# Optimization experiments

Hardware: AMD Instinct MI355X
Metric: run time of the kernel (lower is better)

## Reference

```python
import jax, jax.numpy as jnp
import numpy as np

N, M, KLEN, D_MODEL, H = 256, 256, 128, 256, 8
DK = D_MODEL // H


def _linear_params(key, out_dim, in_dim):
    # torch nn.Linear default init: U(-1/sqrt(in), 1/sqrt(in))
    kw, kb = jax.random.split(key)
    bound = 1.0 / np.sqrt(in_dim)
    W = jax.random.uniform(kw, (out_dim, in_dim), jnp.float32, -bound, bound)
    b = jax.random.uniform(kb, (out_dim,), jnp.float32, -bound, bound)
    return W, b


def setup_inputs() -> dict:
    key = jax.random.key(0)
    ks = jax.random.split(key, 7)
    query = jax.random.normal(ks[0], (N, D_MODEL), jnp.float32)
    key_t = jax.random.normal(ks[1], (M, KLEN, D_MODEL), jnp.float32)
    value = jax.random.normal(ks[2], (M, KLEN, D_MODEL), jnp.float32)
    Wq, bq = _linear_params(ks[3], D_MODEL, D_MODEL)
    Wk, bk = _linear_params(ks[4], D_MODEL, D_MODEL)
    Wv, bv = _linear_params(ks[5], D_MODEL, D_MODEL)
    Wo, bo = _linear_params(ks[6], D_MODEL, D_MODEL)
    return {"query": query, "key": key_t, "value": value,
            "Wq": Wq, "bq": bq, "Wk": Wk, "bk": bk,
            "Wv": Wv, "bv": bv, "Wo": Wo, "bo": bo}


def reference(query, key, value, Wq, bq, Wk, bk, Wv, bv, Wo, bo):
    n = query.shape[0]
    m = key.shape[0]
    # projections (torch Linear: x @ W.T + b)
    q = (query @ Wq.T + bq).reshape(n, H, DK)                      # [n,h,d]
    k = (key @ Wk.T + bk).reshape(m, -1, H, DK).transpose(0, 2, 1, 3)   # [m,h,k,d]
    v = (value @ Wv.T + bv).reshape(m, -1, H, DK).transpose(0, 2, 1, 3)  # [m,h,k,d]
    # cross-batch attention scores: [n,m,h,k]
    scores = jnp.einsum('nhd,mhkd->nmhk', q, k) / np.sqrt(DK).astype(np.float32)
    p_attn = jax.nn.softmax(scores, axis=-1)
    # context: [n,m,h,d] -> [n,m,d_model]
    ctx = jnp.einsum('nmhk,mhkd->nmhd', p_attn, v).reshape(n, m, H * DK)
    return ctx @ Wo.T + bo
```

## Files before the change

kernel.cpp:

```cpp
#include <hip/hip_runtime.h>


typedef unsigned short u16;
typedef unsigned int u32;
typedef __attribute__((ext_vector_type(8))) _Float16 half8;
typedef __attribute__((ext_vector_type(4))) _Float16 half4;
typedef __attribute__((ext_vector_type(4))) float f32x4;
typedef __attribute__((ext_vector_type(4))) unsigned short us4;
typedef __attribute__((ext_vector_type(2))) unsigned int u32x2;

__device__ __forceinline__ u16 f2h(float v) {
  _Float16 h = (_Float16)v;
  return __builtin_bit_cast(u16, h);
}
__device__ __forceinline__ u32 pk2(float lo, float hi) {
  return (u32)f2h(lo) | ((u32)f2h(hi) << 16);
}
__device__ __forceinline__ f32x4 mf16(half8 a, half8 b, f32x4 c) {
  return __builtin_amdgcn_mfma_f32_16x16x32_f16(a, b, c, 0, 0, 0);
}
__device__ __forceinline__ f32x4 mf16k16(half4 a, half4 b, f32x4 c) {
  return __builtin_amdgcn_mfma_f32_16x16x16f16(a, b, c, 0, 0, 0);
}
__device__ __forceinline__ void gload_lds16(const void* g, void* l) {
  __builtin_amdgcn_global_load_lds((const __attribute__((address_space(1))) u32*)g,
                                   (__attribute__((address_space(3))) u32*)l, 16, 0, 0);
}

template<int MODE>
__global__ __launch_bounds__(256) void proj_kernel(const float* __restrict__ X,
                                                   const float* __restrict__ W,
                                                   const float* __restrict__ bias,
                                                   u16* __restrict__ out,
                                                   const float* __restrict__ Wo,
                                                   u16* __restrict__ wof) {
  if (MODE == 0 && blockIdx.x >= 16) {
    int t = (blockIdx.x - 16) * 256 + threadIdx.x;
    int ln = t & 63, jtile = (t >> 6) & 15, h = t >> 10;
    int j = jtile * 16 + (ln & 15);
    int d0 = h * 32 + (ln >> 4) * 8;
    float4 g0 = *(const float4*)(Wo + j * 256 + d0);
    float4 g1 = *(const float4*)(Wo + j * 256 + d0 + 4);
    us4 h0 = { f2h(g0.x), f2h(g0.y), f2h(g0.z), f2h(g0.w) };
    us4 h1 = { f2h(g1.x), f2h(g1.y), f2h(g1.z), f2h(g1.w) };
    *(us4*)(wof + t * 8) = h0;
    *(us4*)(wof + t * 8 + 4) = h1;
    return;
  }
  __shared__ __align__(16) u16 xa[64 * 256];
  __shared__ __align__(16) u16 wa[64 * 256];
  int bid = blockIdx.x;
  int logical;
  if (MODE == 0) {
    logical = bid;
  } else {
    int chunk = gridDim.x >> 3;
    logical = (bid & 7) * chunk + (bid >> 3);
  }
  int rb = logical >> 2, cb = logical & 3;
  int tid = threadIdx.x;

  char* xb = (char*)xa;
  char* wb_ = (char*)wa;
#pragma unroll
  for (int i = 0; i < 16; ++i) {
    int idx = tid + i * 256;
    int row = idx >> 6, c4 = idx & 63;
    int so = (row * 512 + c4 * 8) ^ ((row & 7) << 4);
    float4 gx = *(const float4*)(X + (rb * 64 + row) * 256 + c4 * 4);
    us4 hx = { f2h(gx.x), f2h(gx.y), f2h(gx.z), f2h(gx.w) };
    *(us4*)(xb + so) = hx;
    float4 gw = *(const float4*)(W + (cb * 64 + row) * 256 + c4 * 4);
    us4 hw = { f2h(gw.x), f2h(gw.y), f2h(gw.z), f2h(gw.w) };
    *(us4*)(wb_ + so) = hw;
  }
  __syncthreads();

  int lane = tid & 63, w = tid >> 6;
  int lr = lane & 15, lq = lane >> 4;
  const char* ab = (MODE == 2) ? wb_ : xb;
  const char* bb = (MODE == 2) ? xb : wb_;

  half8 a[8];
#pragma unroll
  for (int kk = 0; kk < 8; ++kk)
    a[kk] = *(const half8*)(ab + (((w * 16 + lr) * 512 + kk * 64 + lq * 16) ^ ((lr & 7) << 4)));

#pragma unroll
  for (int ct = 0; ct < 4; ++ct) {
    f32x4 acc = {0.f, 0.f, 0.f, 0.f};
#pragma unroll
    for (int kk = 0; kk < 8; ++kk) {
      half8 b = *(const half8*)(bb + (((ct * 16 + lr) * 512 + kk * 64 + lq * 16) ^ ((lr & 7) << 4)));
      acc = mf16(a[kk], b, acc);
    }
    if (MODE != 2) {
      int j = cb * 64 + ct * 16 + lr;
      float bj = bias[j];
#pragma unroll
      for (int rr = 0; rr < 4; ++rr) {
        int gr = rb * 64 + w * 16 + lq * 4 + rr;
        float v = acc[rr] + bj;
        if (MODE == 0) {
          out[gr * 256 + j] = f2h(v);
        } else {
          int mm = gr >> 7, kl = gr & 127, hh = j >> 5, d = j & 31;
          out[(mm * 8 + hh) * 4096 + (kl >> 4) * 512 + ((d >> 3) * 16 + (kl & 15)) * 8 + (d & 7)] = f2h(v);
        }
      }
    } else {
#pragma unroll
      for (int rr = 0; rr < 4; ++rr) {
        int j = cb * 64 + w * 16 + lq * 4 + rr;
        float v = acc[rr] + bias[j];
        int gr = rb * 64 + ct * 16 + lr;
        int mm = gr >> 7, kl = gr & 127, hh = j >> 5, d = j & 31;
        int jt = d >> 4, lrp = d & 15, kt = kl >> 4, lqp = (kl >> 2) & 3, e = kl & 3;
        out[(((mm * 8 + hh) * 2 + jt) * 8 + kt) * 256 + (lqp * 16 + lrp) * 4 + e] = f2h(v);
      }
    }
  }
}

__global__ __launch_bounds__(512, 4) void fused_attn_kernel(const u16* __restrict__ qp,
                                                            const u16* __restrict__ kp,
                                                            const u16* __restrict__ vt3,
                                                            const u16* __restrict__ wof,
                                                            const float* __restrict__ bo,
                                                            float* __restrict__ out) {
  __shared__ __align__(16) u16 kbuf[2][4096];
  __shared__ __align__(16) u16 vbuf[2][4096];
  __shared__ __align__(16) u16 cbuf[2][4096];

  const int bid = blockIdx.x;
  const int xcd = bid & 7, idx = bid >> 3;
  const int m = xcd * 32 + (idx >> 1);
  const int nh = idx & 1;
  const int tid = threadIdx.x;
  const int w = tid >> 6, lane = tid & 63;
  const int lr = lane & 15, lq = lane >> 4;
  const int n0 = nh * 128 + w * 16;
  const float SCL2E = 0.25506980508f;

  const char* kg = (const char*)(kp + m * 8 * 4096);
  const char* vg = (const char*)(vt3 + m * 8 * 4096);

  gload_lds16(kg + w * 1024 + lane * 16, (char*)(&kbuf[0][0]) + w * 1024);
  gload_lds16(vg + w * 1024 + lane * 16, (char*)(&vbuf[0][0]) + w * 1024);
  __syncthreads();

  f32x4 accO[2][8];
#pragma unroll
  for (int jt = 0; jt < 2; ++jt)
#pragma unroll
    for (int nb = 0; nb < 8; ++nb) accO[jt][nb] = f32x4{0.f, 0.f, 0.f, 0.f};

  for (int h = 0; h < 8; ++h) {
    const int cur = h & 1;
    char* kb = (char*)(&kbuf[cur][0]);
    char* vb = (char*)(&vbuf[cur][0]);
    char* cb = (char*)(&cbuf[cur][0]);
    if (h < 7) {
      gload_lds16(kg + (h + 1) * 8192 + w * 1024 + lane * 16, (char*)(&kbuf[cur ^ 1][0]) + w * 1024);
      gload_lds16(vg + (h + 1) * 8192 + w * 1024 + lane * 16, (char*)(&vbuf[cur ^ 1][0]) + w * 1024);
    }
    half8 qa = *(const half8*)(qp + (n0 + lr) * 256 + h * 32 + lq * 8);
    f32x4 s[8];
    __builtin_amdgcn_s_setprio(1);
#pragma unroll
    for (int kt = 0; kt < 8; ++kt) {
      half8 ka = *(const half8*)(kb + kt * 1024 + lane * 16);
      f32x4 z = {0.f, 0.f, 0.f, 0.f};
      s[kt] = mf16(ka, qa, z);
    }
    __builtin_amdgcn_s_setprio(0);
    f32x4 m4 = s[0];
#pragma unroll
    for (int kt = 1; kt < 8; ++kt) {
      m4[0] = fmaxf(m4[0], s[kt][0]);
      m4[1] = fmaxf(m4[1], s[kt][1]);
      m4[2] = fmaxf(m4[2], s[kt][2]);
      m4[3] = fmaxf(m4[3], s[kt][3]);
    }
    float mx = fmaxf(fmaxf(m4[0], m4[1]), fmaxf(m4[2], m4[3]));
    mx = fmaxf(mx, __shfl_xor(mx, 16));
    mx = fmaxf(mx, __shfl_xor(mx, 32));
    float sA = 0.f, sB = 0.f;
    half4 pb[8];
#pragma unroll
    for (int kt = 0; kt < 8; ++kt) {
      float p0 = __builtin_amdgcn_exp2f((s[kt][0] - mx) * SCL2E);
      float p1 = __builtin_amdgcn_exp2f((s[kt][1] - mx) * SCL2E);
      float p2 = __builtin_amdgcn_exp2f((s[kt][2] - mx) * SCL2E);
      float p3 = __builtin_amdgcn_exp2f((s[kt][3] - mx) * SCL2E);
      sA += p0 + p1; sB += p2 + p3;
      u32x2 pw = { pk2(p0, p1), pk2(p2, p3) };
      pb[kt] = __builtin_bit_cast(half4, pw);
    }
    float sum = sA + sB;
    sum += __shfl_xor(sum, 16);
    sum += __shfl_xor(sum, 32);
    float inv = 1.0f / sum;
    f32x4 a0 = {0.f, 0.f, 0.f, 0.f}, a1 = {0.f, 0.f, 0.f, 0.f};
    __builtin_amdgcn_s_setprio(1);
#pragma unroll
    for (int kt = 0; kt < 8; ++kt) {
      half4 v0 = *(const half4*)(vb + kt * 512 + lane * 8);
      a0 = mf16k16(v0, pb[kt], a0);
      half4 v1 = *(const half4*)(vb + 4096 + kt * 512 + lane * 8);
      a1 = mf16k16(v1, pb[kt], a1);
    }
    __builtin_amdgcn_s_setprio(0);
    u32x2 c0 = { pk2(a0[0] * inv, a0[1] * inv), pk2(a0[2] * inv, a0[3] * inv) };
    u32x2 c1 = { pk2(a1[0] * inv, a1[1] * inv), pk2(a1[2] * inv, a1[3] * inv) };
    const int cwo = w * 1024 + ((lq >> 1) * 16 + lr) * 16 + (lq & 1) * 8;
    *(u32x2*)(cb + cwo) = c0;
    *(u32x2*)(cb + cwo + 512) = c1;
    __syncthreads();
    half8 wv0 = *(const half8*)(wof + ((h * 16 + w * 2 + 0) * 64 + lane) * 8);
    half8 wv1 = *(const half8*)(wof + ((h * 16 + w * 2 + 1) * 64 + lane) * 8);
    __builtin_amdgcn_s_setprio(1);
#pragma unroll
    for (int nb = 0; nb < 8; ++nb) {
      half8 cf = *(const half8*)(cb + nb * 1024 + lane * 16);
      accO[0][nb] = mf16(wv0, cf, accO[0][nb]);
      accO[1][nb] = mf16(wv1, cf, accO[1][nb]);
    }
    __builtin_amdgcn_s_setprio(0);
  }
#pragma unroll
  for (int jt = 0; jt < 2; ++jt) {
    const int j0 = w * 32 + jt * 16 + lq * 4;
    float4 bv = *(const float4*)(bo + j0);
#pragma unroll
    for (int nb = 0; nb < 8; ++nb) {
      const int n = nh * 128 + nb * 16 + lr;
      float4 r;
      r.x = accO[jt][nb][0] + bv.x;
      r.y = accO[jt][nb][1] + bv.y;
      r.z = accO[jt][nb][2] + bv.z;
      r.w = accO[jt][nb][3] + bv.w;
      *(float4*)(out + (n * 256 + m) * 256 + j0) = r;
    }
  }
}

extern "C" void kernel_launch(void* const* d_in, const int* in_sizes, int n_in,
                              void* d_out, int out_size, void* d_ws, size_t ws_size,
                              hipStream_t stream) {
  (void)in_sizes; (void)n_in; (void)out_size; (void)ws_size;
  const float* query = (const float*)d_in[0];
  const float* key   = (const float*)d_in[1];
  const float* value = (const float*)d_in[2];
  const float* Wq = (const float*)d_in[3];
  const float* bq = (const float*)d_in[4];
  const float* Wk = (const float*)d_in[5];
  const float* bk = (const float*)d_in[6];
  const float* Wv = (const float*)d_in[7];
  const float* bv = (const float*)d_in[8];
  const float* Wo = (const float*)d_in[9];
  const float* bo = (const float*)d_in[10];
  float* out = (float*)d_out;

  u16* ws = (u16*)d_ws;
  u16* kp  = ws;
  u16* vt3 = kp + 8388608;
  u16* qp  = vt3 + 8388608;
  u16* wof = qp + 65536;

  proj_kernel<0><<<48,   256, 0, stream>>>(query, Wq, bq, qp, Wo, wof);
  proj_kernel<1><<<2048, 256, 0, stream>>>(key,   Wk, bk, kp, nullptr, nullptr);
  proj_kernel<2><<<2048, 256, 0, stream>>>(value, Wv, bv, vt3, nullptr, nullptr);
  fused_attn_kernel<<<512, 512, 0, stream>>>(qp, kp, vt3, wof, bo, out);
}
```

Baseline: 85.79 us.

## Pre-convert weights to fp16 fragment layout in a separate kernel

A new kernel converts all four weight matrices to fp16 once, stored in MFMA fragment order. The projection kernels then read weight fragments straight from global memory instead of converting and staging a weight tile in LDS, which halves LDS use and allows higher occupancy. Outputs are written as vectorized 4-element stores in fragment layouts, including a fragment layout for Q. In the attention kernel, the Wo and Q fragment loads are hoisted earlier and the V loads are merged into one 16-byte read. This adds an extra kernel launch, and every block now rereads its weight fragments from global/L2.

```diff
diff --git a/kernel.cpp b/kernel.cpp
--- a/kernel.cpp
+++ b/kernel.cpp
@@ -27,41 +27,42 @@
                                    (__attribute__((address_space(3))) u32*)l, 16, 0, 0);
 }
 
+__global__ __launch_bounds__(256) void wcvt_kernel(const float* __restrict__ Wq,
+                                                   const float* __restrict__ Wk,
+                                                   const float* __restrict__ Wv,
+                                                   const float* __restrict__ Wo,
+                                                   u16* __restrict__ wfq, u16* __restrict__ wfk,
+                                                   u16* __restrict__ wfv, u16* __restrict__ wof) {
+  int t = blockIdx.x * 256 + threadIdx.x;
+  int widx = t >> 13, tl = t & 8191;
+  int ln = tl & 63, kk = (tl >> 6) & 7, jt = tl >> 9;
+  const float* src = widx == 0 ? Wq : widx == 1 ? Wk : widx == 2 ? Wv : Wo;
+  u16* dst = widx == 0 ? wfq : widx == 1 ? wfk : widx == 2 ? wfv : wof;
+  int j = jt * 16 + (ln & 15);
+  int k0 = kk * 32 + (ln >> 4) * 8;
+  float4 g0 = *(const float4*)(src + j * 256 + k0);
+  float4 g1 = *(const float4*)(src + j * 256 + k0 + 4);
+  us4 h0 = { f2h(g0.x), f2h(g0.y), f2h(g0.z), f2h(g0.w) };
+  us4 h1 = { f2h(g1.x), f2h(g1.y), f2h(g1.z), f2h(g1.w) };
+  int idx8 = (widx == 3) ? ((kk * 16 + jt) * 64 + ln)
+                         : ((jt * 8 + kk) * 64 + ln);
+  *(us4*)(dst + idx8 * 8) = h0;
+  *(us4*)(dst + idx8 * 8 + 4) = h1;
+}
+
 template<int MODE>
-__global__ __launch_bounds__(256) void proj_kernel(const float* __restrict__ X,
-                                                   const float* __restrict__ W,
-                                                   const float* __restrict__ bias,
-                                                   u16* __restrict__ out,
-                                                   const float* __restrict__ Wo,
-                                                   u16* __restrict__ wof) {
-  if (MODE == 0 && blockIdx.x >= 16) {
-    int t = (blockIdx.x - 16) * 256 + threadIdx.x;
-    int ln = t & 63, jtile = (t >> 6) & 15, h = t >> 10;
-    int j = jtile * 16 + (ln & 15);
-    int d0 = h * 32 + (ln >> 4) * 8;
-    float4 g0 = *(const float4*)(Wo + j * 256 + d0);
-    float4 g1 = *(const float4*)(Wo + j * 256 + d0 + 4);
-    us4 h0 = { f2h(g0.x), f2h(g0.y), f2h(g0.z), f2h(g0.w) };
-    us4 h1 = { f2h(g1.x), f2h(g1.y), f2h(g1.z), f2h(g1.w) };
-    *(us4*)(wof + t * 8) = h0;
-    *(us4*)(wof + t * 8 + 4) = h1;
-    return;
-  }
+__global__ __launch_bounds__(256, 4) void proj_kernel(const float* __restrict__ X,
+                                                      const u16* __restrict__ wf,
+                                                      const float* __restrict__ bias,
+                                                      u16* __restrict__ out) {
   __shared__ __align__(16) u16 xa[64 * 256];
-  __shared__ __align__(16) u16 wa[64 * 256];
   int bid = blockIdx.x;
   int logical;
-  if (MODE == 0) {
-    logical = bid;
-  } else {
-    int chunk = gridDim.x >> 3;
-    logical = (bid & 7) * chunk + (bid >> 3);
-  }
+  if (MODE == 0) logical = bid;
+  else { int chunk = gridDim.x >> 3; logical = (bid & 7) * chunk + (bid >> 3); }
   int rb = logical >> 2, cb = logical & 3;
   int tid = threadIdx.x;
-
   char* xb = (char*)xa;
-  char* wb_ = (char*)wa;
 #pragma unroll
   for (int i = 0; i < 16; ++i) {
     int idx = tid + i * 256;
@@ -70,59 +71,69 @@
     float4 gx = *(const float4*)(X + (rb * 64 + row) * 256 + c4 * 4);
     us4 hx = { f2h(gx.x), f2h(gx.y), f2h(gx.z), f2h(gx.w) };
     *(us4*)(xb + so) = hx;
-    float4 gw = *(const float4*)(W + (cb * 64 + row) * 256 + c4 * 4);
-    us4 hw = { f2h(gw.x), f2h(gw.y), f2h(gw.z), f2h(gw.w) };
-    *(us4*)(wb_ + so) = hw;
   }
   __syncthreads();
 
   int lane = tid & 63, w = tid >> 6;
   int lr = lane & 15, lq = lane >> 4;
-  const char* ab = (MODE == 2) ? wb_ : xb;
-  const char* bb = (MODE == 2) ? xb : wb_;
-
-  half8 a[8];
-#pragma unroll
-  for (int kk = 0; kk < 8; ++kk)
-    a[kk] = *(const half8*)(ab + (((w * 16 + lr) * 512 + kk * 64 + lq * 16) ^ ((lr & 7) << 4)));
-
-#pragma unroll
-  for (int ct = 0; ct < 4; ++ct) {
-    f32x4 acc = {0.f, 0.f, 0.f, 0.f};
-#pragma unroll
-    for (int kk = 0; kk < 8; ++kk) {
-      half8 b = *(const half8*)(bb + (((ct * 16 + lr) * 512 + kk * 64 + lq * 16) ^ ((lr & 7) << 4)));
-      acc = mf16(a[kk], b, acc);
-    }
-    if (MODE != 2) {
-      int j = cb * 64 + ct * 16 + lr;
+
+  if (MODE == 2) {
+    half8 a[8];
+#pragma unroll
+    for (int kk = 0; kk < 8; ++kk)
+      a[kk] = *(const half8*)(xb + (((w * 16 + lr) * 512 + kk * 64 + lq * 16) ^ ((lr & 7) << 4)));
+#pragma unroll
+    for (int ct = 0; ct < 4; ++ct) {
+      int jtile = cb * 4 + ct;
+      f32x4 acc = {0.f, 0.f, 0.f, 0.f};
+#pragma unroll
+      for (int kk = 0; kk < 8; ++kk) {
+        half8 b = *(const half8*)(wf + ((jtile * 8 + kk) * 64 + lane) * 8);
+        acc = mf16(a[kk], b, acc);
+      }
+      int j = jtile * 16 + lr;
       float bj = bias[j];
-#pragma unroll
-      for (int rr = 0; rr < 4; ++rr) {
-        int gr = rb * 64 + w * 16 + lq * 4 + rr;
-        float v = acc[rr] + bj;
-        if (MODE == 0) {
-          out[gr * 256 + j] = f2h(v);
-        } else {
-          int mm = gr >> 7, kl = gr & 127, hh = j >> 5, d = j & 31;
-          out[(mm * 8 + hh) * 4096 + (kl >> 4) * 512 + ((d >> 3) * 16 + (kl & 15)) * 8 + (d & 7)] = f2h(v);
-        }
+      int h = j >> 5, d = j & 31;
+      int gr0 = rb * 64 + w * 16 + lq * 4;
+      int mm = gr0 >> 7, kl0 = gr0 & 127;
+      int base = (mm * 8 + h) * 4096 + (kl0 >> 4) * 512
+               + ((d & 15) + ((kl0 >> 2) & 3) * 16) * 8 + (d >> 4) * 4;
+      us4 st = { f2h(acc[0] + bj), f2h(acc[1] + bj), f2h(acc[2] + bj), f2h(acc[3] + bj) };
+      *(us4*)(out + base) = st;
+    }
+  } else {
+    int jtile = cb * 4 + w;
+    half8 a[8];
+#pragma unroll
+    for (int kk = 0; kk < 8; ++kk)
+      a[kk] = *(const half8*)(wf + ((jtile * 8 + kk) * 64 + lane) * 8);
+    int j0 = jtile * 16 + lq * 4;
+    float4 bv = *(const float4*)(bias + j0);
+    int h = j0 >> 5, d0 = j0 & 31;
+#pragma unroll
+    for (int ct = 0; ct < 4; ++ct) {
+      f32x4 acc = {0.f, 0.f, 0.f, 0.f};
+#pragma unroll
+      for (int kk = 0; kk < 8; ++kk) {
+        half8 b = *(const half8*)(xb + (((ct * 16 + lr) * 512 + kk * 64 + lq * 16) ^ ((lr & 7) << 4)));
+        acc = mf16(a[kk], b, acc);
       }
-    } else {
-#pragma unroll
-      for (int rr = 0; rr < 4; ++rr) {
-        int j = cb * 64 + w * 16 + lq * 4 + rr;
-        float v = acc[rr] + bias[j];
-        int gr = rb * 64 + ct * 16 + lr;
-        int mm = gr >> 7, kl = gr & 127, hh = j >> 5, d = j & 31;
-        int jt = d >> 4, lrp = d & 15, kt = kl >> 4, lqp = (kl >> 2) & 3, e = kl & 3;
-        out[(((mm * 8 + hh) * 2 + jt) * 8 + kt) * 256 + (lqp * 16 + lrp) * 4 + e] = f2h(v);
+      int gr = rb * 64 + ct * 16 + lr;
+      us4 st = { f2h(acc[0] + bv.x), f2h(acc[1] + bv.y), f2h(acc[2] + bv.z), f2h(acc[3] + bv.w) };
+      if (MODE == 0) {
+        int idx = (((gr >> 4) * 8 + h) * 64 + (d0 >> 3) * 16 + (gr & 15)) * 8 + (d0 & 7);
+        *(us4*)(out + idx) = st;
+      } else {
+        int mm = gr >> 7, kl = gr & 127;
+        int idx = (mm * 8 + h) * 4096 + (kl >> 4) * 512
+                + ((d0 >> 3) * 16 + (kl & 15)) * 8 + (d0 & 7);
+        *(us4*)(out + idx) = st;
       }
     }
   }
 }
 
-__global__ __launch_bounds__(512, 4) void fused_attn_kernel(const u16* __restrict__ qp,
+__global__ __launch_bounds__(512, 4) void fused_attn_kernel(const u16* __restrict__ qf,
                                                             const u16* __restrict__ kp,
                                                             const u16* __restrict__ vt3,
                                                             const u16* __restrict__ wof,
@@ -139,7 +150,6 @@
   const int tid = threadIdx.x;
   const int w = tid >> 6, lane = tid & 63;
   const int lr = lane & 15, lq = lane >> 4;
-  const int n0 = nh * 128 + w * 16;
   const float SCL2E = 0.25506980508f;
 
   const char* kg = (const char*)(kp + m * 8 * 4096);
@@ -164,7 +174,9 @@
       gload_lds16(kg + (h + 1) * 8192 + w * 1024 + lane * 16, (char*)(&kbuf[cur ^ 1][0]) + w * 1024);
       gload_lds16(vg + (h + 1) * 8192 + w * 1024 + lane * 16, (char*)(&vbuf[cur ^ 1][0]) + w * 1024);
     }
-    half8 qa = *(const half8*)(qp + (n0 + lr) * 256 + h * 32 + lq * 8);
+    half8 wv0 = *(const half8*)(wof + ((h * 16 + w * 2 + 0) * 64 + lane) * 8);
+    half8 wv1 = *(const half8*)(wof + ((h * 16 + w * 2 + 1) * 64 + lane) * 8);
+    half8 qa = *(const half8*)(qf + (((nh * 8 + w) * 8 + h) * 64 + lane) * 8);
     f32x4 s[8];
     __builtin_amdgcn_s_setprio(1);
 #pragma unroll
@@ -205,9 +217,10 @@
     __builtin_amdgcn_s_setprio(1);
 #pragma unroll
     for (int kt = 0; kt < 8; ++kt) {
-      half4 v0 = *(const half4*)(vb + kt * 512 + lane * 8);
+      half8 v01 = *(const half8*)(vb + kt * 1024 + lane * 16);
+      half4 v0 = __builtin_shufflevector(v01, v01, 0, 1, 2, 3);
+      half4 v1 = __builtin_shufflevector(v01, v01, 4, 5, 6, 7);
       a0 = mf16k16(v0, pb[kt], a0);
-      half4 v1 = *(const half4*)(vb + 4096 + kt * 512 + lane * 8);
       a1 = mf16k16(v1, pb[kt], a1);
     }
     __builtin_amdgcn_s_setprio(0);
@@ -217,8 +230,6 @@
     *(u32x2*)(cb + cwo) = c0;
     *(u32x2*)(cb + cwo + 512) = c1;
     __syncthreads();
-    half8 wv0 = *(const half8*)(wof + ((h * 16 + w * 2 + 0) * 64 + lane) * 8);
-    half8 wv1 = *(const half8*)(wof + ((h * 16 + w * 2 + 1) * 64 + lane) * 8);
     __builtin_amdgcn_s_setprio(1);
 #pragma unroll
     for (int nb = 0; nb < 8; ++nb) {
@@ -263,13 +274,17 @@
   float* out = (float*)d_out;
 
   u16* ws = (u16*)d_ws;
-  u16* kp  = ws;
-  u16* vt3 = kp + 8388608;
-  u16* qp  = vt3 + 8388608;
-  u16* wof = qp + 65536;
-
-  proj_kernel<0><<<48,   256, 0, stream>>>(query, Wq, bq, qp, Wo, wof);
-  proj_kernel<1><<<2048, 256, 0, stream>>>(key,   Wk, bk, kp, nullptr, nullptr);
-  proj_kernel<2><<<2048, 256, 0, stream>>>(value, Wv, bv, vt3, nullptr, nullptr);
-  fused_attn_kernel<<<512, 512, 0, stream>>>(qp, kp, vt3, wof, bo, out);
-}
+  u16* kfrag = ws;
+  u16* vt3   = kfrag + 8388608;
+  u16* qf    = vt3 + 8388608;
+  u16* wof   = qf + 65536;
+  u16* wfq   = wof + 65536;
+  u16* wfk   = wfq + 65536;
+  u16* wfv   = wfk + 65536;
+
+  wcvt_kernel<<<128, 256, 0, stream>>>(Wq, Wk, Wv, Wo, wfq, wfk, wfv, wof);
+  proj_kernel<0><<<16,   256, 0, stream>>>(query, wfq, bq, qf);
+  proj_kernel<1><<<2048, 256, 0, stream>>>(key,   wfk, bk, kfrag);
+  proj_kernel<2><<<2048, 256, 0, stream>>>(value, wfv, bv, vt3);
+  fused_attn_kernel<<<512, 512, 0, stream>>>(qf, kfrag, vt3, wof, bo, out);
+}
```

Measured after the change: 89.54 us. 1.04x slower.
